# Kernel tuning notes

Measured on AMD Instinct MI355X. Metric: run time of the kernel, lower is better.

## Reference

```python
import jax, jax.numpy as jnp
import numpy as np

VOCAB, EMBED, HIDDEN = 32000, 256, 512
B, T = 8, 512


def setup_inputs() -> dict:
    key = jax.random.key(0)
    ks = jax.random.split(key, 7)
    x = jax.random.randint(ks[0], (B, T), 0, VOCAB)
    emb = jax.random.normal(ks[1], (VOCAB, EMBED), dtype=jnp.float32)
    W_xh = jax.random.normal(ks[2], (EMBED, HIDDEN), dtype=jnp.float32) * 0.01
    W_hh = jax.random.normal(ks[3], (HIDDEN, HIDDEN), dtype=jnp.float32) * 0.01
    b_h = jnp.zeros((HIDDEN,), dtype=jnp.float32)
    # nn.Linear(hidden*2, vocab): weight [vocab, 2*hidden], bias [vocab]
    lim = 1.0 / np.sqrt(2 * HIDDEN)
    fc_w = jax.random.uniform(ks[4], (VOCAB, 2 * HIDDEN), minval=-lim, maxval=lim, dtype=jnp.float32)
    fc_b = jax.random.uniform(ks[5], (VOCAB,), minval=-lim, maxval=lim, dtype=jnp.float32)
    return {"x": x, "emb": emb, "W_xh": W_xh, "W_hh": W_hh, "b_h": b_h, "fc_w": fc_w, "fc_b": fc_b}


def reference(x, emb, W_xh, W_hh, b_h, fc_w, fc_b):
    e = emb[x]  # [B,T,E]
    h0 = jnp.zeros((x.shape[0], W_hh.shape[0]), dtype=e.dtype)

    def step(h, xt):  # xt: [B,E]
        h = jnp.tanh(xt @ W_xh + h @ W_hh + b_h)
        return h, h

    _, H = jax.lax.scan(step, h0, jnp.swapaxes(e, 0, 1))  # H: [T,B,Hd]
    H = jnp.swapaxes(H, 0, 1)  # [B,T,Hd]
    # full (non-causal) dot-product self-attention over hidden states
    scores = jnp.einsum('bth,bsh->bts', H, H)  # [B,T,T]
    attn = jax.nn.softmax(scores, axis=-1)
    ctx = jnp.einsum('bts,bsh->bth', attn, H)  # [B,T,Hd]
    combined = jnp.concatenate([H, ctx], axis=-1)  # [B,T,2Hd]
    return combined @ fc_w.T + fc_b  # [B,T,V]
```

## Files before the change

kernel.cpp:

```cpp
#include <hip/hip_runtime.h>

typedef unsigned int u32;
typedef unsigned short u16;
typedef short bf16x8 __attribute__((ext_vector_type(8)));
typedef float f32x4 __attribute__((ext_vector_type(4)));

#define DEV __device__ __forceinline__

DEV u16 f2bf(float f) {
  u32 u = __builtin_bit_cast(u32, f);
  u += 0x7fffu + ((u >> 16) & 1u);
  return (u16)(u >> 16);
}
DEV float bf2f(u16 b) { u32 u = ((u32)b) << 16; return __builtin_bit_cast(float, u); }

DEV float dot2bf(float acc, u32 w, u32 h) {
  asm("v_dot2_f32_bf16 %0, %1, %2, %0" : "+v"(acc) : "v"(w), "v"(h));
  return acc;
}

DEV void gload16(const void* g, void* l) {
  __builtin_amdgcn_global_load_lds(
      (__attribute__((address_space(1))) void*)(void*)g,
      (__attribute__((address_space(3))) void*)l, 16, 0, 0);
}

__global__ void k_prep_fcw(const float* __restrict__ w, u16* __restrict__ o, int n4) {
  int i = blockIdx.x * blockDim.x + threadIdx.x;
  int stride = gridDim.x * blockDim.x;
  for (; i < n4; i += stride) {
    float4 v = ((const float4*)w)[i];
    ushort4 r; r.x = f2bf(v.x); r.y = f2bf(v.y); r.z = f2bf(v.z); r.w = f2bf(v.w);
    ((ushort4*)o)[i] = r;
  }
}

#define PREG 184
#define PLQ  18

__global__ void k_prep_whh(const float* __restrict__ w, u32* __restrict__ wr, u32* __restrict__ wq) {
  int idx = blockIdx.x * 256 + threadIdx.x;
  int p = idx >> 9, j = idx & 511;
  u32 word = (u32)f2bf(w[(2 * p) * 512 + j]) | ((u32)f2bf(w[(2 * p + 1) * 512 + j]) << 16);
  if (p < PREG) wr[p * 512 + j] = word;
  else { int d = p - PREG; wq[((d >> 2) * 512 + j) * 4 + (d & 3)] = word; }
}

__global__ __launch_bounds__(256) void k_embx(
    const int* __restrict__ x, const float* __restrict__ emb,
    const float* __restrict__ wxh, const float* __restrict__ bh,
    float* __restrict__ X) {
  __shared__ float sA[64][65];
  __shared__ __align__(16) float sB[64][68];
  int tid = threadIdx.x;
  int row0 = blockIdx.x * 64, col0 = blockIdx.y * 64;
  int tx = tid & 15, ty = tid >> 4;
  f32x4 acc[4] = {};
  for (int kc = 0; kc < 256; kc += 64) {
    __syncthreads();
#pragma unroll
    for (int i = 0; i < 4; ++i) {
      int f = i * 256 + tid;
      int r = f >> 4, c4 = (f & 15) * 4;
      int xr = x[row0 + r];
      float4 v = *(const float4*)&emb[(size_t)xr * 256 + kc + c4];
      sA[r][c4 + 0] = v.x; sA[r][c4 + 1] = v.y; sA[r][c4 + 2] = v.z; sA[r][c4 + 3] = v.w;
      float4 u = *(const float4*)&wxh[(size_t)(kc + r) * 512 + col0 + c4];
      *(float4*)&sB[r][c4] = u;
    }
    __syncthreads();
#pragma unroll
    for (int e = 0; e < 64; ++e) {
      f32x4 bv = *(const f32x4*)&sB[e][tx * 4];
      float a0 = sA[ty * 4 + 0][e], a1 = sA[ty * 4 + 1][e];
      float a2 = sA[ty * 4 + 2][e], a3 = sA[ty * 4 + 3][e];
      acc[0] += a0 * bv; acc[1] += a1 * bv; acc[2] += a2 * bv; acc[3] += a3 * bv;
    }
  }
  f32x4 bh4 = *(const f32x4*)&bh[col0 + tx * 4];
#pragma unroll
  for (int a = 0; a < 4; ++a) {
    f32x4 r = acc[a] + bh4;
    *(f32x4*)&X[(size_t)(row0 + ty * 4 + a) * 512 + col0 + tx * 4] = r;
  }
}

__global__ __launch_bounds__(512)
__attribute__((amdgpu_waves_per_eu(2, 2)))
void k_rnn(
    const u32* __restrict__ Wr, const u32* __restrict__ Wq,
    const float* __restrict__ X,
    u16* __restrict__ Hb16 ) {
  __shared__ __align__(16) u32 wl[PLQ * 512 * 4];
  __shared__ __align__(16) u32 hHI[2][256];
  __shared__ __align__(16) u32 hLO[2][256];
  int j = threadIdx.x;
  int b = blockIdx.x;
  u32 wreg[PREG];
#pragma unroll
  for (int p = 0; p < PREG; ++p) wreg[p] = Wr[p * 512 + j];
#pragma unroll
  for (int q = 0; q < PLQ; ++q)
    *(uint4*)&wl[(q * 512 + j) * 4] = *(const uint4*)&Wq[(q * 512 + j) * 4];
  if (j < 256) { hHI[0][j] = 0u; hLO[0][j] = 0u; }
  const float* Xb = X + (size_t)b * 512 * 512;
  u16* Hb = Hb16 + (size_t)b * 512 * 1024;
  __syncthreads();
  int cur = 0;
  float xv = Xb[j];
  for (int t = 0; t < 512; ++t) {
    int tn = t < 511 ? t + 1 : 511;
    float xnext = Xb[tn * 512 + j];
    float a0 = 0.f, a1 = 0.f, a2 = 0.f, a3 = 0.f;
    const u32* hbH = hHI[cur];
    const u32* hbL = hLO[cur];
#pragma unroll
    for (int c = 0; c < PREG / 4; ++c) {
      uint4 hH = *(const uint4*)&hbH[c * 4];
      uint4 hL = *(const uint4*)&hbL[c * 4];
      a0 = dot2bf(dot2bf(a0, wreg[c * 4 + 0], hH.x), wreg[c * 4 + 0], hL.x);
      a1 = dot2bf(dot2bf(a1, wreg[c * 4 + 1], hH.y), wreg[c * 4 + 1], hL.y);
      a2 = dot2bf(dot2bf(a2, wreg[c * 4 + 2], hH.z), wreg[c * 4 + 2], hL.z);
      a3 = dot2bf(dot2bf(a3, wreg[c * 4 + 3], hH.w), wreg[c * 4 + 3], hL.w);
    }
#pragma unroll
    for (int q = 0; q < PLQ; ++q) {
      uint4 wv = *(const uint4*)&wl[(q * 512 + j) * 4];
      uint4 hH = *(const uint4*)&hbH[PREG + q * 4];
      uint4 hL = *(const uint4*)&hbL[PREG + q * 4];
      a0 = dot2bf(dot2bf(a0, wv.x, hH.x), wv.x, hL.x);
      a1 = dot2bf(dot2bf(a1, wv.y, hH.y), wv.y, hL.y);
      a2 = dot2bf(dot2bf(a2, wv.z, hH.z), wv.z, hL.z);
      a3 = dot2bf(dot2bf(a3, wv.w, hH.w), wv.w, hL.w);
    }
    float z = xv + ((a0 + a1) + (a2 + a3));
    float ez = __expf(2.f * z);
    float h = 1.f - 2.f / (ez + 1.f);
    u16 hi = f2bf(h);
    u16 lo = f2bf(h - bf2f(hi));
    Hb[t * 1024 + j] = hi;
    ((u16*)hHI[cur ^ 1])[j] = hi;
    ((u16*)hLO[cur ^ 1])[j] = lo;
    __syncthreads();
    cur ^= 1;
    xv = xnext;
  }
}

template <int BF16OUT, int BIAS, int BF32B>
__global__ __launch_bounds__(256) void k_gemm_bt(
    const u16* __restrict__ A, int lda, long long aStr,
    const void* __restrict__ Bt_, int ldb, long long bStr,
    void* __restrict__ Cv, int ldc, long long cStr,
    int numMt, int numNt, int K, const float* __restrict__ bias) {
  __shared__ __align__(16) u16 lA[128 * 64];
  __shared__ __align__(16) u16 lB[128 * 64];
  int tid = threadIdx.x;
  int lane = tid & 63, wid = tid >> 6;
  int nwg = gridDim.x, wg = blockIdx.x;
  int q = nwg >> 3;
  int swz = (wg & 7) * q + (wg >> 3);
  int gm = numMt < 8 ? numMt : 8;
  int perg = gm * numNt;
  int grp = swz / perg;
  int rem = swz - grp * perg;
  int mt = grp * gm + rem % gm;
  int nt = rem / gm;
  int mrow = mt * 128, ncol = nt * 128;
  long long batch = blockIdx.y;
  A += batch * aStr;
  const u16* Bh = (const u16*)Bt_ + (BF32B ? 0 : batch * bStr);
  const float* Bf = (const float*)Bt_ + (BF32B ? batch * bStr : 0);
  float* Cf = (float*)Cv + batch * cStr;
  u16* Ch = (u16*)Cv + batch * cStr;

  f32x4 acc[4][4] = {};
  int wr = wid >> 1, wc = wid & 1;
  int lr = lane & 15, lk = (lane >> 4) * 8;

  for (int kt = 0; kt < K; kt += 64) {
    __syncthreads();
#pragma unroll
    for (int i = 0; i < 4; ++i) {
      int chunk = wid * 4 + i;
      int idx = chunk * 64 + lane;
      int r = idx >> 3, c = (idx & 7) * 8;
      gload16(&A[(size_t)(mrow + r) * lda + kt + c], &lA[chunk * 512]);
    }
    if constexpr (!BF32B) {
#pragma unroll
      for (int i = 0; i < 4; ++i) {
        int chunk = wid * 4 + i;
        int idx = chunk * 64 + lane;
        int r = idx >> 3, c = (idx & 7) * 8;
        gload16(&Bh[(size_t)(ncol + r) * ldb + kt + c], &lB[chunk * 512]);
      }
    } else {
#pragma unroll
      for (int u = 0; u < 8; ++u) {
        int flat = u * 1024 + tid * 4;
        int r = flat >> 6, c = flat & 63;
        float4 v = *(const float4*)&Bf[(size_t)(ncol + r) * ldb + kt + c];
        uint2 pk;
        pk.x = (u32)f2bf(v.x) | ((u32)f2bf(v.y) << 16);
        pk.y = (u32)f2bf(v.z) | ((u32)f2bf(v.w) << 16);
        *(uint2*)&lB[r * 64 + c] = pk;
      }
    }
    __syncthreads();
#pragma unroll
    for (int ks = 0; ks < 2; ++ks) {
      bf16x8 aF[4], bF[4];
#pragma unroll
      for (int mi = 0; mi < 4; ++mi)
        aF[mi] = *(const bf16x8*)&lA[(wr * 64 + mi * 16 + lr) * 64 + ks * 32 + lk];
#pragma unroll
      for (int ni = 0; ni < 4; ++ni)
        bF[ni] = *(const bf16x8*)&lB[(wc * 64 + ni * 16 + lr) * 64 + ks * 32 + lk];
#pragma unroll
      for (int mi = 0; mi < 4; ++mi)
#pragma unroll
        for (int ni = 0; ni < 4; ++ni)
          acc[mi][ni] = __builtin_amdgcn_mfma_f32_16x16x32_bf16(aF[mi], bF[ni], acc[mi][ni], 0, 0, 0);
    }
  }
  int rq = (lane >> 4) * 4;
#pragma unroll
  for (int ni = 0; ni < 4; ++ni) {
    int col = ncol + wc * 64 + ni * 16 + lr;
    float bv = BIAS ? bias[col] : 0.f;
#pragma unroll
    for (int mi = 0; mi < 4; ++mi) {
      int row = mrow + wr * 64 + mi * 16 + rq;
#pragma unroll
      for (int qq = 0; qq < 4; ++qq) {
        float v = acc[mi][ni][qq] + bv;
        if (BF16OUT) Ch[(size_t)(row + qq) * ldc + col] = f2bf(v);
        else         Cf[(size_t)(row + qq) * ldc + col] = v;
      }
    }
  }
}

__global__ __launch_bounds__(256) void k_softmax(const float* __restrict__ S, u16* __restrict__ P) {
  int wid = threadIdx.x >> 6, lane = threadIdx.x & 63;
  int row = blockIdx.x * 4 + wid;
  const float* sr = S + (size_t)row * 512;
  f32x4 v0 = *(const f32x4*)&sr[lane * 4];
  f32x4 v1 = *(const f32x4*)&sr[256 + lane * 4];
  float m = fmaxf(fmaxf(fmaxf(v0.x, v0.y), fmaxf(v0.z, v0.w)),
                  fmaxf(fmaxf(v1.x, v1.y), fmaxf(v1.z, v1.w)));
#pragma unroll
  for (int o = 32; o; o >>= 1) m = fmaxf(m, __shfl_xor(m, o, 64));
  f32x4 e0, e1;
  e0.x = __expf(v0.x - m); e0.y = __expf(v0.y - m); e0.z = __expf(v0.z - m); e0.w = __expf(v0.w - m);
  e1.x = __expf(v1.x - m); e1.y = __expf(v1.y - m); e1.z = __expf(v1.z - m); e1.w = __expf(v1.w - m);
  float s = (e0.x + e0.y + e0.z + e0.w) + (e1.x + e1.y + e1.z + e1.w);
#pragma unroll
  for (int o = 32; o; o >>= 1) s += __shfl_xor(s, o, 64);
  float inv = 1.f / s;
  ushort4 o0, o1;
  o0.x = f2bf(e0.x * inv); o0.y = f2bf(e0.y * inv); o0.z = f2bf(e0.z * inv); o0.w = f2bf(e0.w * inv);
  o1.x = f2bf(e1.x * inv); o1.y = f2bf(e1.y * inv); o1.z = f2bf(e1.z * inv); o1.w = f2bf(e1.w * inv);
  *(ushort4*)&P[(size_t)row * 512 + lane * 4] = o0;
  *(ushort4*)&P[(size_t)row * 512 + 256 + lane * 4] = o1;
}

__global__ __launch_bounds__(256) void k_transpose(const u16* __restrict__ Hsrc, u16* __restrict__ HT) {
  __shared__ __align__(16) u16 tile[64][72];
  int b = blockIdx.z;
  int sb = blockIdx.x * 64, hb = blockIdx.y * 64;
  int tid = threadIdx.x;
#pragma unroll
  for (int i = 0; i < 4; ++i) {
    int f = i * 256 + tid; int r = f >> 4, c4 = (f & 15) * 4;
    ushort4 v = *(const ushort4*)&Hsrc[((size_t)(b * 512 + sb + r)) * 1024 + hb + c4];
    *(ushort4*)&tile[r][c4] = v;
  }
  __syncthreads();
#pragma unroll
  for (int i = 0; i < 4; ++i) {
    int f = i * 256 + tid; int h = f >> 4, s4 = (f & 15) * 4;
    ushort4 v;
    v.x = tile[s4 + 0][h]; v.y = tile[s4 + 1][h]; v.z = tile[s4 + 2][h]; v.w = tile[s4 + 3][h];
    *(ushort4*)&HT[((size_t)(b * 512 + hb + h)) * 512 + sb + s4] = v;
  }
}

extern "C" void kernel_launch(void* const* d_in, const int* in_sizes, int n_in,
                              void* d_out, int out_size, void* d_ws, size_t ws_size,
                              hipStream_t stream) {
  const int*   x   = (const int*)d_in[0];
  const float* emb = (const float*)d_in[1];
  const float* wxh = (const float*)d_in[2];
  const float* whh = (const float*)d_in[3];
  const float* bh  = (const float*)d_in[4];
  const float* fcw = (const float*)d_in[5];
  const float* fcb = (const float*)d_in[6];
  float* out = (float*)d_out;

  char* ws = (char*)d_ws;
  u32* Wr  = (u32*)ws;
  u32* Wq  = (u32*)(ws + 376832);
  u16* comb = (u16*)(ws + 524288);
  u16* fcwb = (u16*)(ws + 524288 + 8388608);
  bool bigws = ws_size >= (size_t)(524288 + 8388608 + 65536000);
  char* ob = (char*)d_out;
  float* X  = (float*)ob;
  float* S  = (float*)(ob + 8388608);
  u16*   P  = (u16*)(ob + 16777216);
  u16*   HT = (u16*)(ob + 20971520);

  k_prep_whh<<<dim3(512), dim3(256), 0, stream>>>(whh, Wr, Wq);
  k_embx<<<dim3(64, 8), dim3(256), 0, stream>>>(x, emb, wxh, bh, X);
  if (bigws)
    k_prep_fcw<<<dim3(2048), dim3(256), 0, stream>>>(fcw, fcwb, 8192000);
  k_rnn<<<dim3(8), dim3(512), 0, stream>>>(Wr, Wq, X, comb);
  k_gemm_bt<0, 0, 0><<<dim3(16, 8), dim3(256), 0, stream>>>(
      comb, 1024, 512LL * 1024, comb, 1024, 512LL * 1024,
      (void*)S, 512, 512LL * 512, 4, 4, 512, (const float*)nullptr);
  k_softmax<<<dim3(1024), dim3(256), 0, stream>>>(S, P);
  k_transpose<<<dim3(8, 8, 8), dim3(256), 0, stream>>>(comb, HT);
  k_gemm_bt<1, 0, 0><<<dim3(16, 8), dim3(256), 0, stream>>>(
      P, 512, 512LL * 512, HT, 512, 512LL * 512,
      (void*)(comb + 512), 1024, 512LL * 1024, 4, 4, 512, (const float*)nullptr);
  if (bigws)
    k_gemm_bt<0, 1, 0><<<dim3(8000), dim3(256), 0, stream>>>(
        comb, 1024, 0LL, fcwb, 1024, 0LL,
        (void*)out, 32000, 0LL, 32, 250, 1024, fcb);
  else
    k_gemm_bt<0, 1, 1><<<dim3(8000), dim3(256), 0, stream>>>(
        comb, 1024, 0LL, fcw, 1024, 0LL,
        (void*)out, 32000, 0LL, 32, 250, 1024, fcb);
}
```

Baseline: 1.797 ms.

## Split RNN recurrence K-dimension across two thread halves per hidden unit

The recurrent kernel now launches 1024 threads per batch block, splitting the 512-long reduction over the hidden state into two halves of 256, each with 128 packed weight pairs (96 in registers, 32 in LDS). The second half writes its partial sum to shared memory and the first half combines, applies tanh and writes h. This halves per-thread serial dot work and register pressure per step to shorten the sequential latency, at the cost of an extra barrier per timestep and an idle half during the activation.

```diff
diff --git a/kernel.cpp b/kernel.cpp
--- a/kernel.cpp
+++ b/kernel.cpp
@@ -35,15 +35,17 @@
   }
 }
 
-#define PREG 184
-#define PLQ  18
+#define PW_REG 96
+#define PW_LQ  8
 
 __global__ void k_prep_whh(const float* __restrict__ w, u32* __restrict__ wr, u32* __restrict__ wq) {
   int idx = blockIdx.x * 256 + threadIdx.x;
   int p = idx >> 9, j = idx & 511;
   u32 word = (u32)f2bf(w[(2 * p) * 512 + j]) | ((u32)f2bf(w[(2 * p + 1) * 512 + j]) << 16);
-  if (p < PREG) wr[p * 512 + j] = word;
-  else { int d = p - PREG; wq[((d >> 2) * 512 + j) * 4 + (d & 3)] = word; }
+  int s = p >> 7, lp = p & 127;
+  int col = s * 512 + j;
+  if (lp < PW_REG) wr[lp * 1024 + col] = word;
+  else { int d = lp - PW_REG; wq[((d >> 2) * 1024 + col) * 4 + (d & 3)] = word; }
 }
 
 __global__ __launch_bounds__(256) void k_embx(
@@ -85,37 +87,38 @@
   }
 }
 
-__global__ __launch_bounds__(512)
-__attribute__((amdgpu_waves_per_eu(2, 2)))
-void k_rnn(
+__global__ __launch_bounds__(1024) void k_rnn(
     const u32* __restrict__ Wr, const u32* __restrict__ Wq,
     const float* __restrict__ X,
     u16* __restrict__ Hb16 ) {
-  __shared__ __align__(16) u32 wl[PLQ * 512 * 4];
+  __shared__ __align__(16) u32 wl[PW_LQ * 1024 * 4];
   __shared__ __align__(16) u32 hHI[2][256];
   __shared__ __align__(16) u32 hLO[2][256];
-  int j = threadIdx.x;
+  __shared__ float ppart[512];
+  int tid = threadIdx.x;
+  int s = tid >> 9, j = tid & 511;
   int b = blockIdx.x;
-  u32 wreg[PREG];
-#pragma unroll
-  for (int p = 0; p < PREG; ++p) wreg[p] = Wr[p * 512 + j];
-#pragma unroll
-  for (int q = 0; q < PLQ; ++q)
-    *(uint4*)&wl[(q * 512 + j) * 4] = *(const uint4*)&Wq[(q * 512 + j) * 4];
-  if (j < 256) { hHI[0][j] = 0u; hLO[0][j] = 0u; }
+  u32 wreg[PW_REG];
+#pragma unroll
+  for (int p = 0; p < PW_REG; ++p) wreg[p] = Wr[p * 1024 + tid];
+#pragma unroll
+  for (int q = 0; q < PW_LQ; ++q)
+    *(uint4*)&wl[(q * 1024 + tid) * 4] = *(const uint4*)&Wq[(q * 1024 + tid) * 4];
+  if (tid < 256) { hHI[0][tid] = 0u; hLO[0][tid] = 0u; }
   const float* Xb = X + (size_t)b * 512 * 512;
   u16* Hb = Hb16 + (size_t)b * 512 * 1024;
   __syncthreads();
   int cur = 0;
-  float xv = Xb[j];
+  int hoff = s << 7;
+  float xv = (s == 0) ? Xb[j] : 0.f;
   for (int t = 0; t < 512; ++t) {
-    int tn = t < 511 ? t + 1 : 511;
-    float xnext = Xb[tn * 512 + j];
+    float xnext = 0.f;
+    if (s == 0) { int tn = t < 511 ? t + 1 : 511; xnext = Xb[tn * 512 + j]; }
     float a0 = 0.f, a1 = 0.f, a2 = 0.f, a3 = 0.f;
-    const u32* hbH = hHI[cur];
-    const u32* hbL = hLO[cur];
-#pragma unroll
-    for (int c = 0; c < PREG / 4; ++c) {
+    const u32* hbH = hHI[cur] + hoff;
+    const u32* hbL = hLO[cur] + hoff;
+#pragma unroll
+    for (int c = 0; c < PW_REG / 4; ++c) {
       uint4 hH = *(const uint4*)&hbH[c * 4];
       uint4 hL = *(const uint4*)&hbL[c * 4];
       a0 = dot2bf(dot2bf(a0, wreg[c * 4 + 0], hH.x), wreg[c * 4 + 0], hL.x);
@@ -124,23 +127,28 @@
       a3 = dot2bf(dot2bf(a3, wreg[c * 4 + 3], hH.w), wreg[c * 4 + 3], hL.w);
     }
 #pragma unroll
-    for (int q = 0; q < PLQ; ++q) {
-      uint4 wv = *(const uint4*)&wl[(q * 512 + j) * 4];
-      uint4 hH = *(const uint4*)&hbH[PREG + q * 4];
-      uint4 hL = *(const uint4*)&hbL[PREG + q * 4];
+    for (int q = 0; q < PW_LQ; ++q) {
+      uint4 wv = *(const uint4*)&wl[(q * 1024 + tid) * 4];
+      uint4 hH = *(const uint4*)&hbH[PW_REG + q * 4];
+      uint4 hL = *(const uint4*)&hbL[PW_REG + q * 4];
       a0 = dot2bf(dot2bf(a0, wv.x, hH.x), wv.x, hL.x);
       a1 = dot2bf(dot2bf(a1, wv.y, hH.y), wv.y, hL.y);
       a2 = dot2bf(dot2bf(a2, wv.z, hH.z), wv.z, hL.z);
       a3 = dot2bf(dot2bf(a3, wv.w, hH.w), wv.w, hL.w);
     }
-    float z = xv + ((a0 + a1) + (a2 + a3));
-    float ez = __expf(2.f * z);
-    float h = 1.f - 2.f / (ez + 1.f);
-    u16 hi = f2bf(h);
-    u16 lo = f2bf(h - bf2f(hi));
-    Hb[t * 1024 + j] = hi;
-    ((u16*)hHI[cur ^ 1])[j] = hi;
-    ((u16*)hLO[cur ^ 1])[j] = lo;
+    float a = (a0 + a1) + (a2 + a3);
+    if (s) ppart[j] = a;
+    __syncthreads();
+    if (!s) {
+      float z = xv + a + ppart[j];
+      float ez = __expf(2.f * z);
+      float h = 1.f - 2.f / (ez + 1.f);
+      u16 hi = f2bf(h);
+      u16 lo = f2bf(h - bf2f(hi));
+      Hb[t * 1024 + j] = hi;
+      ((u16*)hHI[cur ^ 1])[j] = hi;
+      ((u16*)hLO[cur ^ 1])[j] = lo;
+    }
     __syncthreads();
     cur ^= 1;
     xv = xnext;
@@ -301,7 +309,7 @@
 
   char* ws = (char*)d_ws;
   u32* Wr  = (u32*)ws;
-  u32* Wq  = (u32*)(ws + 376832);
+  u32* Wq  = (u32*)(ws + 393216);
   u16* comb = (u16*)(ws + 524288);
   u16* fcwb = (u16*)(ws + 524288 + 8388608);
   bool bigws = ws_size >= (size_t)(524288 + 8388608 + 65536000);
@@ -315,7 +323,7 @@
   k_embx<<<dim3(64, 8), dim3(256), 0, stream>>>(x, emb, wxh, bh, X);
   if (bigws)
     k_prep_fcw<<<dim3(2048), dim3(256), 0, stream>>>(fcw, fcwb, 8192000);
-  k_rnn<<<dim3(8), dim3(512), 0, stream>>>(Wr, Wq, X, comb);
+  k_rnn<<<dim3(8), dim3(1024), 0, stream>>>(Wr, Wq, X, comb);
   k_gemm_bt<0, 0, 0><<<dim3(16, 8), dim3(256), 0, stream>>>(
       comb, 1024, 512LL * 1024, comb, 1024, 512LL * 1024,
       (void*)S, 512, 512LL * 512, 4, 4, 512, (const float*)nullptr);
```

After: 2.016 ms. +12.2%, slower.

## Add 256x256-tile 8-wave pipelined GEMM for the vocab projection

Applied to the files above, without the earlier changes.

Replaces the 128x128-tile GEMM used for the large output projection with a new kernel that uses 256x256 tiles, 8 waves per block, double-buffered LDS staged in half-K chunks with XOR swizzling, and global loads interleaved with the MFMA phases. The goal is more data reuse per LDS load and better overlap of memory with compute on the dominant vocab GEMM. In exchange it uses 128KB of LDS per block and many accumulator registers, which may limit occupancy. The wave-grouped tile remap is intended to improve L2 locality.

```diff
diff --git a/kernel.cpp b/kernel.cpp
--- a/kernel.cpp
+++ b/kernel.cpp
@@ -242,6 +242,116 @@
   }
 }
 
+DEV void stage_half(const u16* __restrict__ G, int ldg, int grow0, int kcol0,
+                    u16* region, int w, int lane) {
+#pragma unroll
+  for (int jj = 0; jj < 2; ++jj) {
+    int fb = jj * 512 + w * 64;
+    int f = fb + lane;
+    int r = f >> 2, s = f & 3;
+    int c = (s ^ (r & 3)) * 8;
+    gload16(&G[(size_t)(grow0 + r) * ldg + kcol0 + c], region + (size_t)fb * 8);
+  }
+}
+DEV bf16x8 lds_frag(const u16* region, int r, int lq) {
+  return *(const bf16x8*)&region[r * 32 + ((lq ^ (r & 3)) * 8)];
+}
+
+__global__ __launch_bounds__(512, 2) void k_gemm8(
+    const u16* __restrict__ A, int lda,
+    const u16* __restrict__ B, int ldb,
+    float* __restrict__ C, int ldc,
+    int numMt, int numNt, int K, const float* __restrict__ bias) {
+  __shared__ __align__(16) u16 lds8[65536];
+  int tid = threadIdx.x;
+  int lane = tid & 63, wid = tid >> 6;
+  int w = wid, wm = wid >> 2, wn = wid & 3;
+  int lr = lane & 15, lq = lane >> 4;
+  int nwg = gridDim.x, wg = blockIdx.x;
+  int qd = nwg >> 3;
+  int swz = (wg & 7) * qd + (wg >> 3);
+  int gm = numMt < 8 ? numMt : 8;
+  int perg = gm * numNt;
+  int grp = swz / perg;
+  int rem = swz - grp * perg;
+  int mt = grp * gm + rem % gm;
+  int nt = rem / gm;
+  int mrow = mt * 256, ncol = nt * 256;
+  int NT = K >> 6;
+
+#define REGION(buf, op, kh) (lds8 + (((buf) * 2 + (op)) * 2 + (kh)) * 8192)
+
+  f32x4 acc[8][4];
+#pragma unroll
+  for (int mi = 0; mi < 8; ++mi)
+#pragma unroll
+    for (int ni = 0; ni < 4; ++ni) acc[mi][ni] = (f32x4){0.f, 0.f, 0.f, 0.f};
+
+  stage_half(A, lda, mrow, 0,  REGION(0, 0, 0), w, lane);
+  stage_half(B, ldb, ncol, 0,  REGION(0, 1, 0), w, lane);
+  stage_half(A, lda, mrow, 32, REGION(0, 0, 1), w, lane);
+  stage_half(B, ldb, ncol, 32, REGION(0, 1, 1), w, lane);
+  stage_half(A, lda, mrow, 64, REGION(1, 0, 0), w, lane);
+  stage_half(B, ldb, ncol, 64, REGION(1, 1, 0), w, lane);
+  asm volatile("s_waitcnt vmcnt(4)" ::: "memory");
+  __builtin_amdgcn_s_barrier();
+  asm volatile("" ::: "memory");
+
+  for (int T = 0; T < NT; ++T) {
+    int buf = T & 1;
+    int s12 = (T + 1 < NT), s34 = (T + 2 < NT);
+#pragma unroll
+    for (int ph = 0; ph < 4; ++ph) {
+      int ch = ph & 1, ks = ph >> 1;
+      const u16* Ar = REGION(buf, 0, ks);
+      const u16* Br = REGION(buf, 1, ks);
+      bf16x8 aF[8], bF[2];
+#pragma unroll
+      for (int mi = 0; mi < 8; ++mi)
+        aF[mi] = lds_frag(Ar, wm * 128 + mi * 16 + lr, lq);
+#pragma unroll
+      for (int nl = 0; nl < 2; ++nl)
+        bF[nl] = lds_frag(Br, wn * 64 + (ch * 2 + nl) * 16 + lr, lq);
+      if (ph == 0) { if (s12) stage_half(A, lda, mrow, (T + 1) * 64 + 32, REGION(buf ^ 1, 0, 1), w, lane); }
+      if (ph == 1) { if (s12) stage_half(B, ldb, ncol, (T + 1) * 64 + 32, REGION(buf ^ 1, 1, 1), w, lane); }
+      if (ph == 2) { if (s34) stage_half(A, lda, mrow, (T + 2) * 64,      REGION(buf, 0, 0),     w, lane); }
+      if (ph == 3) { if (s34) stage_half(B, ldb, ncol, (T + 2) * 64,      REGION(buf, 1, 0),     w, lane); }
+      asm volatile("" ::: "memory");
+      __builtin_amdgcn_s_barrier();
+      asm volatile("s_waitcnt lgkmcnt(0)" ::: "memory");
+      __builtin_amdgcn_sched_barrier(0);
+      __builtin_amdgcn_s_setprio(1);
+#pragma unroll
+      for (int mi = 0; mi < 8; ++mi) {
+        acc[mi][ch * 2 + 0] = __builtin_amdgcn_mfma_f32_16x16x32_bf16(aF[mi], bF[0], acc[mi][ch * 2 + 0], 0, 0, 0);
+        acc[mi][ch * 2 + 1] = __builtin_amdgcn_mfma_f32_16x16x32_bf16(aF[mi], bF[1], acc[mi][ch * 2 + 1], 0, 0, 0);
+      }
+      __builtin_amdgcn_s_setprio(0);
+      if (ph == 3) {
+        if (T >= NT - 2) asm volatile("s_waitcnt vmcnt(0)" ::: "memory");
+        else             asm volatile("s_waitcnt vmcnt(4)" ::: "memory");
+      }
+      asm volatile("" ::: "memory");
+      __builtin_amdgcn_s_barrier();
+      asm volatile("" ::: "memory");
+    }
+  }
+#undef REGION
+
+#pragma unroll
+  for (int mi = 0; mi < 8; ++mi) {
+    int row0 = mrow + wm * 128 + mi * 16 + lq * 4;
+#pragma unroll
+    for (int ni = 0; ni < 4; ++ni) {
+      int col = ncol + wn * 64 + ni * 16 + lr;
+      float bv = bias[col];
+#pragma unroll
+      for (int rg = 0; rg < 4; ++rg)
+        C[(size_t)(row0 + rg) * ldc + col] = acc[mi][ni][rg] + bv;
+    }
+  }
+}
+
 __global__ __launch_bounds__(256) void k_softmax(const float* __restrict__ S, u16* __restrict__ P) {
   int wid = threadIdx.x >> 6, lane = threadIdx.x & 63;
   int row = blockIdx.x * 4 + wid;
@@ -325,9 +435,8 @@
       P, 512, 512LL * 512, HT, 512, 512LL * 512,
       (void*)(comb + 512), 1024, 512LL * 1024, 4, 4, 512, (const float*)nullptr);
   if (bigws)
-    k_gemm_bt<0, 1, 0><<<dim3(8000), dim3(256), 0, stream>>>(
-        comb, 1024, 0LL, fcwb, 1024, 0LL,
-        (void*)out, 32000, 0LL, 32, 250, 1024, fcb);
+    k_gemm8<<<dim3(2000), dim3(512), 0, stream>>>(
+        comb, 1024, fcwb, 1024, out, 32000, 16, 125, 1024, fcb);
   else
     k_gemm_bt<0, 1, 1><<<dim3(8000), dim3(256), 0, stream>>>(
         comb, 1024, 0LL, fcw, 1024, 0LL,
```

Measured after the change: 1.692 ms. 5.8% less time.
